# Kernel tuning notes

Hardware: AMD Instinct MI355X
Metric: run time of the kernel (lower is better)

## Reference

```python
import jax, jax.numpy as jnp
import numpy as np

DIM = 3072
NUM_HEADS = 24
HEAD_DIM = 128
INNER = NUM_HEADS * HEAD_DIM
EPS = 1e-5


def _layernorm(x, eps=EPS):
    # affine-free LayerNorm over the last (head_dim) axis
    mu = jnp.mean(x, axis=-1, keepdims=True)
    var = jnp.mean(jnp.square(x - mu), axis=-1, keepdims=True)
    return (x - mu) * jax.lax.rsqrt(var + eps)


def _rope_interleaved(x, cos, sin):
    # x: (B, S_img, H, D); cos/sin: (S_img, D//2). Non-neox (interleaved) style.
    x1 = x[..., 0::2]
    x2 = x[..., 1::2]
    c = cos[None, :, None, :]
    s = sin[None, :, None, :]
    o1 = x1 * c - x2 * s
    o2 = x2 * c + x1 * s
    return jnp.stack([o1, o2], axis=-1).reshape(x.shape)


def setup_inputs() -> dict:
    key = jax.random.key(0)
    ks = jax.random.split(key, 8)
    B, S_txt, S_img = 1, 256, 2048
    hidden_states = jax.random.normal(ks[0], (B, S_img, DIM), dtype=jnp.float32)
    encoder_hidden_states = jax.random.normal(ks[1], (B, S_txt, DIM), dtype=jnp.float32)
    cos = jax.random.uniform(ks[2], (S_img, HEAD_DIM // 2), dtype=jnp.float32)
    sin = jax.random.uniform(ks[3], (S_img, HEAD_DIM // 2), dtype=jnp.float32)
    Wqkv = jax.random.normal(ks[4], (DIM, 3 * INNER), dtype=jnp.float32) * (DIM ** -0.5)
    bqkv = jnp.zeros((3 * INNER,), dtype=jnp.float32)
    Wout = jax.random.normal(ks[5], (INNER, DIM), dtype=jnp.float32) * (INNER ** -0.5)
    bout = jnp.zeros((DIM,), dtype=jnp.float32)
    return {
        "hidden_states": hidden_states,
        "encoder_hidden_states": encoder_hidden_states,
        "cos": cos,
        "sin": sin,
        "Wqkv": Wqkv,
        "bqkv": bqkv,
        "Wout": Wout,
        "bout": bout,
        "text_seq_length": 256,
    }


def reference(hidden_states, encoder_hidden_states, cos, sin, Wqkv, bqkv, Wout, bout, text_seq_length):
    T = text_seq_length
    x = jnp.concatenate([encoder_hidden_states, hidden_states], axis=1)  # (B, S, dim)
    B, S, _ = x.shape
    qkv = x @ Wqkv + bqkv  # (B, S, 3*inner)
    q, k, v = jnp.split(qkv, 3, axis=-1)
    q = q.reshape(B, S, NUM_HEADS, HEAD_DIM)
    k = k.reshape(B, S, NUM_HEADS, HEAD_DIM)
    v = v.reshape(B, S, NUM_HEADS, HEAD_DIM)
    q = _layernorm(q)
    k = _layernorm(k)
    # partial RoPE: only on image-token slice
    q = jnp.concatenate([q[:, :T], _rope_interleaved(q[:, T:], cos, sin)], axis=1)
    k = jnp.concatenate([k[:, :T], _rope_interleaved(k[:, T:], cos, sin)], axis=1)
    scale = 1.0 / (HEAD_DIM ** 0.5)
    scores = jnp.einsum("bqhd,bkhd->bhqk", q, k) * scale
    probs = jax.nn.softmax(scores, axis=-1)
    out = jnp.einsum("bhqk,bkhd->bqhd", probs, v)
    out = out.reshape(B, S, INNER)
    out = out @ Wout + bout
    encoder_out = out[:, :T, :]
    hidden_out = out[:, T:, :]
    return (hidden_out, encoder_out)
```

## Files before the change

kernel.cpp:

```cpp
#include <hip/hip_runtime.h>

#define DIMC 3072
#define NH 24
#define HD 128
#define QKV_N 9216
#define S_TXT 256
#define S_IMG 2048
#define S_TOT 2304

typedef _Float16 f16x8 __attribute__((ext_vector_type(8)));
typedef _Float16 f16x4 __attribute__((ext_vector_type(4)));
typedef _Float16 f16x2 __attribute__((ext_vector_type(2)));
typedef float f32x4 __attribute__((ext_vector_type(4)));

#define MFMA(A, B, C) __builtin_amdgcn_mfma_f32_16x16x32_f16(A, B, C, 0, 0, 0)

#define QSCALE (0.08838834764831845f * 1.4426950408889634f)

__device__ __forceinline__ void gl2lds16(const _Float16* g, _Float16* l) {
    __builtin_amdgcn_global_load_lds(
        (const __attribute__((address_space(1))) unsigned int*)g,
        (__attribute__((address_space(3))) unsigned int*)l,
        16, 0, 0);
}

__global__ __launch_bounds__(256) void split_x(
    const float* __restrict__ enc, const float* __restrict__ hid,
    _Float16* __restrict__ xh)
{
    const int s = blockIdx.x;
    const float* src = (s < S_TXT) ? enc + (size_t)s * DIMC
                                   : hid + (size_t)(s - S_TXT) * DIMC;
    const int t = threadIdx.x;
#pragma unroll
    for (int it = 0; it < 3; ++it) {
        const int i = (it * 256 + t) * 4;
        float4 v = *(const float4*)(src + i);
        f16x4 hv;
        hv.x = (_Float16)v.x; hv.y = (_Float16)v.y;
        hv.z = (_Float16)v.z; hv.w = (_Float16)v.w;
        *(f16x4*)(xh + (size_t)s * DIMC + i) = hv;
    }
}

__global__ __launch_bounds__(256) void transpose_w_hi(
    const float* __restrict__ W, const int ldw, _Float16* __restrict__ Th)
{
    __shared__ float T[64][68];
    const int n0 = blockIdx.x * 64, k0 = blockIdx.y * 64;
    const int t = threadIdx.x;
    {
        const int r = t >> 2, c4 = (t & 3) * 16;
#pragma unroll
        for (int j = 0; j < 4; ++j) {
            float4 v = *(const float4*)(W + (size_t)(k0 + r) * ldw + n0 + c4 + j * 4);
            *(float4*)&T[r][c4 + j * 4] = v;
        }
    }
    __syncthreads();
    const int nr = t >> 2, kp = (t & 3) * 16;
    f16x8 hv0, hv1;
#pragma unroll
    for (int j = 0; j < 8; ++j) hv0[j] = (_Float16)T[kp + j][nr];
#pragma unroll
    for (int j = 0; j < 8; ++j) hv1[j] = (_Float16)T[kp + 8 + j][nr];
    _Float16* dh = Th + (size_t)(n0 + nr) * DIMC + k0 + kp;
    *(f16x8*)(dh) = hv0; *(f16x8*)(dh + 8) = hv1;
}

template <int REMAP>
__global__ __launch_bounds__(256) void gemm_f16_lds(
    const _Float16* __restrict__ Ah, const _Float16* __restrict__ Bh,
    const float* __restrict__ bias, float* __restrict__ C,
    const int nblk_m, const int ldc)
{
    __shared__ __attribute__((aligned(16))) _Float16 Ash[128 * 32];
    __shared__ __attribute__((aligned(16))) _Float16 Bsh[128 * 32];

    const int cpx = (int)gridDim.x >> 3;
    const int wgid = (blockIdx.x & 7) * cpx + (blockIdx.x >> 3);
    const int bm = (wgid % nblk_m) * 128;
    const int bn = (wgid / nblk_m) * 128;

    const int tid = threadIdx.x;
    const int l = tid & 63, w = tid >> 6;
    const int wr = w >> 1, wc = w & 1;
    const int lr = l & 15, g = l >> 4;

    const int srow0 = w * 32 + (l >> 2);
    const int srow1 = srow0 + 16;
    const int skp0 = (((l & 3) ^ ((srow0 >> 1) & 3)) * 8);
    const int skp1 = (((l & 3) ^ ((srow1 >> 1) & 3)) * 8);
    const _Float16* gA0 = Ah + (size_t)(bm + srow0) * DIMC + skp0;
    const _Float16* gA1 = Ah + (size_t)(bm + srow1) * DIMC + skp1;
    const _Float16* gB0 = Bh + (size_t)(bn + srow0) * DIMC + skp0;
    const _Float16* gB1 = Bh + (size_t)(bn + srow1) * DIMC + skp1;
    _Float16* lA0 = &Ash[(w * 32) * 32];
    _Float16* lA1 = &Ash[(w * 32 + 16) * 32];
    _Float16* lB0 = &Bsh[(w * 32) * 32];
    _Float16* lB1 = &Bsh[(w * 32 + 16) * 32];

    int aoff[4], boff[4];
#pragma unroll
    for (int i = 0; i < 4; ++i) {
        const int ra = wr * 64 + i * 16 + lr;
        const int rb = wc * 64 + i * 16 + lr;
        aoff[i] = ra * 32 + ((g ^ ((ra >> 1) & 3)) * 8);
        boff[i] = rb * 32 + ((g ^ ((rb >> 1) & 3)) * 8);
    }

    f32x4 acc[4][4] = {};

    for (int k0 = 0; k0 < DIMC; k0 += 32) {
        gl2lds16(gA0 + k0, lA0);
        gl2lds16(gA1 + k0, lA1);
        gl2lds16(gB0 + k0, lB0);
        gl2lds16(gB1 + k0, lB1);
        __syncthreads();

        f16x8 bhf[4];
#pragma unroll
        for (int ni = 0; ni < 4; ++ni)
            bhf[ni] = *(const f16x8*)&Bsh[boff[ni]];
#pragma unroll
        for (int mi = 0; mi < 4; ++mi) {
            f16x8 ahf = *(const f16x8*)&Ash[aoff[mi]];
#pragma unroll
            for (int ni = 0; ni < 4; ++ni)
                acc[mi][ni] = MFMA(ahf, bhf[ni], acc[mi][ni]);
        }
        __syncthreads();
    }

#pragma unroll
    for (int mi = 0; mi < 4; ++mi)
#pragma unroll
        for (int ni = 0; ni < 4; ++ni) {
            const int cl = bn + wc * 64 + ni * 16 + lr;
            const float bv = bias[cl];
#pragma unroll
            for (int e = 0; e < 4; ++e) {
                const int r = bm + wr * 64 + mi * 16 + g * 4 + e;
                if (REMAP) {
                    const int gr = (r < S_TXT) ? (S_IMG + r) : (r - S_TXT);
                    C[(size_t)gr * DIMC + cl] = acc[mi][ni][e] + bv;
                } else {
                    C[(size_t)r * ldc + cl] = acc[mi][ni][e] + bv;
                }
            }
        }
}

__global__ __launch_bounds__(256) void ln_rope_split(
    const float* __restrict__ qkv,
    const float* __restrict__ cost, const float* __restrict__ sint,
    _Float16* __restrict__ Qh, _Float16* __restrict__ Kh)
{
    const int wave = threadIdx.x >> 6;
    const int lane = threadIdx.x & 63;
    const int task = blockIdx.x * 4 + wave;
    const int s = task / 48;
    const int rem = task % 48;
    const int qk = rem / 24;
    const int h = rem % 24;

    const float* p = qkv + (size_t)s * QKV_N + qk * DIMC + h * HD;
    float2 x = *(const float2*)(p + lane * 2);

    float sum = x.x + x.y;
    float sq = x.x * x.x + x.y * x.y;
#pragma unroll
    for (int off = 1; off < 64; off <<= 1) {
        sum += __shfl_xor(sum, off, 64);
        sq  += __shfl_xor(sq, off, 64);
    }
    const float mu = sum * (1.0f / 128.0f);
    const float var = sq * (1.0f / 128.0f) - mu * mu;
    const float rstd = rsqrtf(var + 1e-5f);
    float y0 = (x.x - mu) * rstd;
    float y1 = (x.y - mu) * rstd;

    if (s >= S_TXT) {
        const int ip = s - S_TXT;
        const float c = cost[ip * 64 + lane];
        const float sn = sint[ip * 64 + lane];
        const float o0 = y0 * c - y1 * sn;
        const float o1 = y1 * c + y0 * sn;
        y0 = o0; y1 = o1;
    }
    if (qk == 0) { y0 *= QSCALE; y1 *= QSCALE; }

    const size_t off = ((size_t)h * S_TOT + s) * HD + lane * 2;
    f16x2 hv; hv.x = (_Float16)y0; hv.y = (_Float16)y1;
    *(f16x2*)((qk ? Kh : Qh) + off) = hv;
}

__global__ __launch_bounds__(256) void v_split_transpose(
    const float* __restrict__ qkv, _Float16* __restrict__ Vth)
{
    __shared__ float T[64][132];
    const int h = blockIdx.y;
    const int s0 = blockIdx.x * 64;
    const int t = threadIdx.x;
    {
        const int sl = t >> 2, dp = (t & 3) * 32;
#pragma unroll
        for (int j = 0; j < 8; ++j) {
            float4 v = *(const float4*)(qkv + (size_t)(s0 + sl) * QKV_N + 2 * DIMC + h * HD + dp + j * 4);
            *(float4*)&T[sl][dp + j * 4] = v;
        }
    }
    __syncthreads();
    const int d = t >> 1, sh = (t & 1) * 32;
    f16x8 hv[4];
#pragma unroll
    for (int ss = 0; ss < 32; ++ss)
        hv[ss >> 3][ss & 7] = (_Float16)T[sh + ss][d];
    _Float16* bh = Vth + ((size_t)h * HD + d) * S_TOT + s0 + sh;
#pragma unroll
    for (int j = 0; j < 4; ++j)
        *(f16x8*)(bh + j * 8) = hv[j];
}

__global__ __launch_bounds__(512) void attn_mfma(
    const _Float16* __restrict__ Qg, const _Float16* __restrict__ Kg,
    const _Float16* __restrict__ Vg, _Float16* __restrict__ aoh)
{
    __shared__ __attribute__((aligned(16))) _Float16 Ksh[4 * 64 * 32];
    __shared__ __attribute__((aligned(16))) _Float16 Vsh[128 * 64];
    __shared__ __attribute__((aligned(16))) _Float16 Pah[8 * 16 * 64];

    const int wgid = ((int)blockIdx.x & 7) * 54 + ((int)blockIdx.x >> 3);
    const int h = wgid / 18;
    const int q0 = (wgid % 18) * 128;
    const int tid = threadIdx.x;
    const int w = tid >> 6, l = tid & 63;
    const int lr = l & 15, g = l >> 4;

    const int qrow = q0 + w * 16 + lr;
    const _Float16* qb = Qg + ((size_t)h * S_TOT + qrow) * HD + g * 8;
    f16x8 qh[4];
#pragma unroll
    for (int db = 0; db < 4; ++db)
        qh[db] = *(const f16x8*)(qb + db * 32);

    f32x4 o[8] = {};
    float mrow = -3.0e38f, lrow = 0.0f;

    const int kxr = (lr >> 1) & 3;
    const int px  = lr & 7;
    int ksl[4];
#pragma unroll
    for (int db = 0; db < 4; ++db) ksl[db] = (g ^ kxr ^ db) * 8;
    const int vs0 = (g ^ px) * 8;
    const int vs1 = ((4 + g) ^ px) * 8;

    const int kkv = tid >> 3, kd = tid & 7;
    const int kdb = kd >> 1, kg0 = (kd & 1) * 2;
    const int kx = (kkv >> 1) & 3;
    const int kbase = kdb * 2048 + kkv * 32;
    const int vd = tid >> 2, vh = tid & 3;
    const int vx = vd & 7;
    const int vbase = vd * 64;
    const int vg0 = vh * 2;
    const _Float16* gK = Kg + ((size_t)h * S_TOT + kkv) * HD + kd * 16;
    const _Float16* gV = Vg + ((size_t)h * HD + vd) * S_TOT + vh * 16;

    uint4 rK0, rK1, rV0, rV1;
#define LOADKV(kv0) { \
    rK0 = *(const uint4*)(gK + (size_t)(kv0) * HD);     rK1 = *(const uint4*)(gK + (size_t)(kv0) * HD + 8); \
    rV0 = *(const uint4*)(gV + (kv0));                  rV1 = *(const uint4*)(gV + (kv0) + 8); }

    LOADKV(0);

    for (int kb = 0; kb < S_TOT / 64; ++kb) {
        __syncthreads();
        *(uint4*)&Ksh[kbase + (((kg0 + 0) ^ kx ^ kdb) * 8)] = rK0;
        *(uint4*)&Ksh[kbase + (((kg0 + 1) ^ kx ^ kdb) * 8)] = rK1;
        *(uint4*)&Vsh[vbase + (((vg0 + 0) ^ vx) * 8)] = rV0;
        *(uint4*)&Vsh[vbase + (((vg0 + 1) ^ vx) * 8)] = rV1;
        __syncthreads();
        if (kb + 1 < S_TOT / 64) LOADKV((kb + 1) * 64);

        f32x4 sT[4] = {};
        __builtin_amdgcn_s_setprio(1);
#pragma unroll
        for (int db = 0; db < 4; ++db)
#pragma unroll
            for (int mf = 0; mf < 4; ++mf) {
                f16x8 kf = *(const f16x8*)&Ksh[db * 2048 + (mf * 16 + lr) * 32 + ksl[db]];
                sT[mf] = MFMA(kf, qh[db], sT[mf]);
            }
        __builtin_amdgcn_s_setprio(0);

        float pm = -3.0e38f;
#pragma unroll
        for (int mf = 0; mf < 4; ++mf)
#pragma unroll
            for (int e = 0; e < 4; ++e)
                pm = fmaxf(pm, sT[mf][e]);
        pm = fmaxf(pm, __shfl_xor(pm, 16, 64));
        pm = fmaxf(pm, __shfl_xor(pm, 32, 64));

        if (__any(pm > mrow + 11.0f)) {
            const float mnew = fmaxf(mrow, pm);
            const float alpha = exp2f(mrow - mnew);
            lrow *= alpha;
            mrow = mnew;
            const float a0 = __shfl(alpha, g * 4 + 0, 64);
            const float a1 = __shfl(alpha, g * 4 + 1, 64);
            const float a2 = __shfl(alpha, g * 4 + 2, 64);
            const float a3 = __shfl(alpha, g * 4 + 3, 64);
#pragma unroll
            for (int df = 0; df < 8; ++df) {
                o[df][0] *= a0; o[df][1] *= a1; o[df][2] *= a2; o[df][3] *= a3;
            }
        }

        float rs = 0.0f;
        float ex_[4][4];
#pragma unroll
        for (int mf = 0; mf < 4; ++mf)
#pragma unroll
            for (int e = 0; e < 4; ++e) {
                const float pv = exp2f(sT[mf][e] - mrow);
                ex_[mf][e] = pv;
                rs += pv;
            }
        rs += __shfl_xor(rs, 16, 64);
        rs += __shfl_xor(rs, 32, 64);
        lrow += rs;

        {
            const int pbase = w * 1024 + lr * 64;
#pragma unroll
            for (int mf = 0; mf < 4; ++mf) {
                const int slot = ((mf * 2 + (g >> 1)) ^ px) * 8 + (g & 1) * 4;
                f16x2 t0; t0.x = (_Float16)ex_[mf][0]; t0.y = (_Float16)ex_[mf][1];
                f16x2 t1; t1.x = (_Float16)ex_[mf][2]; t1.y = (_Float16)ex_[mf][3];
                *(f16x2*)&Pah[pbase + slot]     = t0;
                *(f16x2*)&Pah[pbase + slot + 2] = t1;
            }
        }

        f16x8 pa0 = *(const f16x8*)&Pah[w * 1024 + lr * 64 + vs0];
        f16x8 pa1 = *(const f16x8*)&Pah[w * 1024 + lr * 64 + vs1];
        __builtin_amdgcn_s_setprio(1);
#pragma unroll
        for (int df = 0; df < 8; ++df) {
            f16x8 vf0 = *(const f16x8*)&Vsh[(df * 16 + lr) * 64 + vs0];
            f16x8 vf1 = *(const f16x8*)&Vsh[(df * 16 + lr) * 64 + vs1];
            o[df] = MFMA(pa0, vf0, o[df]);
            o[df] = MFMA(pa1, vf1, o[df]);
        }
        __builtin_amdgcn_s_setprio(0);
    }
#undef LOADKV

    const float inv = 1.0f / lrow;
    const float b0 = __shfl(inv, g * 4 + 0, 64);
    const float b1 = __shfl(inv, g * 4 + 1, 64);
    const float b2 = __shfl(inv, g * 4 + 2, 64);
    const float b3 = __shfl(inv, g * 4 + 3, 64);
    const float bb[4] = {b0, b1, b2, b3};
#pragma unroll
    for (int df = 0; df < 8; ++df)
#pragma unroll
        for (int e = 0; e < 4; ++e) {
            const int r = q0 + w * 16 + g * 4 + e;
            aoh[(size_t)r * DIMC + h * HD + df * 16 + lr] = (_Float16)(o[df][e] * bb[e]);
        }
}

extern "C" void kernel_launch(void* const* d_in, const int* in_sizes, int n_in,
                              void* d_out, int out_size, void* d_ws, size_t ws_size,
                              hipStream_t stream)
{
    const float* hid  = (const float*)d_in[0];
    const float* enc  = (const float*)d_in[1];
    const float* cost = (const float*)d_in[2];
    const float* sint = (const float*)d_in[3];
    const float* Wqkv = (const float*)d_in[4];
    const float* bqkv = (const float*)d_in[5];
    const float* Wout = (const float*)d_in[6];
    const float* bout = (const float*)d_in[7];
    float* out = (float*)d_out;

    char* ws = (char*)d_ws;
    float*    qkv  = (float*)(ws + 0);
    _Float16* aoh  = (_Float16*)(ws + 0);
    _Float16* xh   = (_Float16*)(ws + 84934656);
    _Float16* Qh   = (_Float16*)(ws + 84934656);
    _Float16* Kh   = (_Float16*)(ws + 99090432);
    _Float16* Wth  = (_Float16*)(ws + 113246208);
    _Float16* Vth  = (_Float16*)(ws + 113246208);
    _Float16* W2h  = (_Float16*)(ws + 132120576);

    split_x<<<S_TOT, 256, 0, stream>>>(enc, hid, xh);
    transpose_w_hi<<<dim3(144, 48), 256, 0, stream>>>(Wqkv, QKV_N, Wth);
    gemm_f16_lds<0><<<18 * 72, 256, 0, stream>>>(xh, Wth, bqkv, qkv, 18, QKV_N);
    transpose_w_hi<<<dim3(48, 48), 256, 0, stream>>>(Wout, DIMC, W2h);
    ln_rope_split<<<(S_TOT * 48) / 4, 256, 0, stream>>>(qkv, cost, sint, Qh, Kh);
    v_split_transpose<<<dim3(36, 24), 256, 0, stream>>>(qkv, Vth);
    attn_mfma<<<432, 512, 0, stream>>>(Qh, Kh, Vth, aoh);
    gemm_f16_lds<1><<<18 * 24, 256, 0, stream>>>(aoh, W2h, bout, out, 18, DIMC);
}
```

Measured before the change: 411.3 us.

## Fuse QKV split and V transpose into GEMM epilogue writing fp16

The QKV GEMM epilogue now writes Q and K as fp16 in head-major layout and V transposed, instead of writing a full fp32 qkv buffer. The separate V transpose kernel is removed, and LayerNorm plus RoPE now runs in place on the fp16 Q and K. This removes the fp32 write and re-read of roughly 85MB of intermediate data. In exchange, LayerNorm statistics are computed from fp16-rounded values, which adds precision loss, and the scattered 2-byte epilogue stores for Q and K may coalesce poorly.

```diff
diff --git a/kernel.cpp b/kernel.cpp
--- a/kernel.cpp
+++ b/kernel.cpp
@@ -68,19 +68,19 @@
     *(f16x8*)(dh) = hv0; *(f16x8*)(dh + 8) = hv1;
 }
 
-template <int REMAP>
-__global__ __launch_bounds__(256) void gemm_f16_lds(
+__global__ __launch_bounds__(256) void gemm_qkv(
     const _Float16* __restrict__ Ah, const _Float16* __restrict__ Bh,
-    const float* __restrict__ bias, float* __restrict__ C,
-    const int nblk_m, const int ldc)
+    const float* __restrict__ bias,
+    _Float16* __restrict__ Qh, _Float16* __restrict__ Kh,
+    _Float16* __restrict__ Vt)
 {
     __shared__ __attribute__((aligned(16))) _Float16 Ash[128 * 32];
     __shared__ __attribute__((aligned(16))) _Float16 Bsh[128 * 32];
 
     const int cpx = (int)gridDim.x >> 3;
     const int wgid = (blockIdx.x & 7) * cpx + (blockIdx.x >> 3);
-    const int bm = (wgid % nblk_m) * 128;
-    const int bn = (wgid / nblk_m) * 128;
+    const int bm = (wgid % 18) * 128;
+    const int bn = (wgid / 18) * 128;
 
     const int tid = threadIdx.x;
     const int l = tid & 63, w = tid >> 6;
@@ -132,6 +132,107 @@
         __syncthreads();
     }
 
+    const int nb = bn >> 7;
+    const int typ = nb / NH;
+    const int h = nb % NH;
+
+    if (typ == 2) {
+#pragma unroll
+        for (int mi = 0; mi < 4; ++mi) {
+            const int sbase = bm + wr * 64 + mi * 16 + g * 4;
+#pragma unroll
+            for (int ni = 0; ni < 4; ++ni) {
+                const int col = wc * 64 + ni * 16 + lr;
+                const float bv = bias[bn + col];
+                f16x4 vv;
+                vv.x = (_Float16)(acc[mi][ni][0] + bv);
+                vv.y = (_Float16)(acc[mi][ni][1] + bv);
+                vv.z = (_Float16)(acc[mi][ni][2] + bv);
+                vv.w = (_Float16)(acc[mi][ni][3] + bv);
+                *(f16x4*)&Vt[((size_t)h * HD + col) * S_TOT + sbase] = vv;
+            }
+        }
+    } else {
+        _Float16* dst = (typ ? Kh : Qh) + (size_t)h * S_TOT * HD;
+#pragma unroll
+        for (int mi = 0; mi < 4; ++mi)
+#pragma unroll
+            for (int ni = 0; ni < 4; ++ni) {
+                const int col = wc * 64 + ni * 16 + lr;
+                const float bv = bias[bn + col];
+#pragma unroll
+                for (int e = 0; e < 4; ++e) {
+                    const int r = bm + wr * 64 + mi * 16 + g * 4 + e;
+                    dst[(size_t)r * HD + col] = (_Float16)(acc[mi][ni][e] + bv);
+                }
+            }
+    }
+}
+
+template <int REMAP>
+__global__ __launch_bounds__(256) void gemm_f16_lds(
+    const _Float16* __restrict__ Ah, const _Float16* __restrict__ Bh,
+    const float* __restrict__ bias, float* __restrict__ C,
+    const int nblk_m, const int ldc)
+{
+    __shared__ __attribute__((aligned(16))) _Float16 Ash[128 * 32];
+    __shared__ __attribute__((aligned(16))) _Float16 Bsh[128 * 32];
+
+    const int cpx = (int)gridDim.x >> 3;
+    const int wgid = (blockIdx.x & 7) * cpx + (blockIdx.x >> 3);
+    const int bm = (wgid % nblk_m) * 128;
+    const int bn = (wgid / nblk_m) * 128;
+
+    const int tid = threadIdx.x;
+    const int l = tid & 63, w = tid >> 6;
+    const int wr = w >> 1, wc = w & 1;
+    const int lr = l & 15, g = l >> 4;
+
+    const int srow0 = w * 32 + (l >> 2);
+    const int srow1 = srow0 + 16;
+    const int skp0 = (((l & 3) ^ ((srow0 >> 1) & 3)) * 8);
+    const int skp1 = (((l & 3) ^ ((srow1 >> 1) & 3)) * 8);
+    const _Float16* gA0 = Ah + (size_t)(bm + srow0) * DIMC + skp0;
+    const _Float16* gA1 = Ah + (size_t)(bm + srow1) * DIMC + skp1;
+    const _Float16* gB0 = Bh + (size_t)(bn + srow0) * DIMC + skp0;
+    const _Float16* gB1 = Bh + (size_t)(bn + srow1) * DIMC + skp1;
+    _Float16* lA0 = &Ash[(w * 32) * 32];
+    _Float16* lA1 = &Ash[(w * 32 + 16) * 32];
+    _Float16* lB0 = &Bsh[(w * 32) * 32];
+    _Float16* lB1 = &Bsh[(w * 32 + 16) * 32];
+
+    int aoff[4], boff[4];
+#pragma unroll
+    for (int i = 0; i < 4; ++i) {
+        const int ra = wr * 64 + i * 16 + lr;
+        const int rb = wc * 64 + i * 16 + lr;
+        aoff[i] = ra * 32 + ((g ^ ((ra >> 1) & 3)) * 8);
+        boff[i] = rb * 32 + ((g ^ ((rb >> 1) & 3)) * 8);
+    }
+
+    f32x4 acc[4][4] = {};
+
+    for (int k0 = 0; k0 < DIMC; k0 += 32) {
+        gl2lds16(gA0 + k0, lA0);
+        gl2lds16(gA1 + k0, lA1);
+        gl2lds16(gB0 + k0, lB0);
+        gl2lds16(gB1 + k0, lB1);
+        __syncthreads();
+
+        f16x8 bhf[4];
+#pragma unroll
+        for (int ni = 0; ni < 4; ++ni)
+            bhf[ni] = *(const f16x8*)&Bsh[boff[ni]];
+#pragma unroll
+        for (int mi = 0; mi < 4; ++mi) {
+            f16x8 ahf = *(const f16x8*)&Ash[aoff[mi]];
+#pragma unroll
+            for (int ni = 0; ni < 4; ++ni)
+                acc[mi][ni] = MFMA(ahf, bhf[ni], acc[mi][ni]);
+        }
+        __syncthreads();
+    }
+
 #pragma unroll
     for (int mi = 0; mi < 4; ++mi)
 #pragma unroll
@@ -151,10 +252,9 @@
         }
 }
 
-__global__ __launch_bounds__(256) void ln_rope_split(
-    const float* __restrict__ qkv,
-    const float* __restrict__ cost, const float* __restrict__ sint,
-    _Float16* __restrict__ Qh, _Float16* __restrict__ Kh)
+__global__ __launch_bounds__(256) void ln_rope_inplace(
+    _Float16* __restrict__ Qh, _Float16* __restrict__ Kh,
+    const float* __restrict__ cost, const float* __restrict__ sint)
 {
     const int wave = threadIdx.x >> 6;
     const int lane = threadIdx.x & 63;
@@ -164,11 +264,12 @@
     const int qk = rem / 24;
     const int h = rem % 24;
 
-    const float* p = qkv + (size_t)s * QKV_N + qk * DIMC + h * HD;
-    float2 x = *(const float2*)(p + lane * 2);
-
-    float sum = x.x + x.y;
-    float sq = x.x * x.x + x.y * x.y;
+    _Float16* p = (qk ? Kh : Qh) + ((size_t)h * S_TOT + s) * HD + lane * 2;
+    f16x2 xv = *(const f16x2*)p;
+    float x0 = (float)xv.x, x1 = (float)xv.y;
+
+    float sum = x0 + x1;
+    float sq = x0 * x0 + x1 * x1;
 #pragma unroll
     for (int off = 1; off < 64; off <<= 1) {
         sum += __shfl_xor(sum, off, 64);
@@ -177,8 +278,8 @@
     const float mu = sum * (1.0f / 128.0f);
     const float var = sq * (1.0f / 128.0f) - mu * mu;
     const float rstd = rsqrtf(var + 1e-5f);
-    float y0 = (x.x - mu) * rstd;
-    float y1 = (x.y - mu) * rstd;
+    float y0 = (x0 - mu) * rstd;
+    float y1 = (x1 - mu) * rstd;
 
     if (s >= S_TXT) {
         const int ip = s - S_TXT;
@@ -190,36 +291,8 @@
     }
     if (qk == 0) { y0 *= QSCALE; y1 *= QSCALE; }
 
-    const size_t off = ((size_t)h * S_TOT + s) * HD + lane * 2;
     f16x2 hv; hv.x = (_Float16)y0; hv.y = (_Float16)y1;
-    *(f16x2*)((qk ? Kh : Qh) + off) = hv;
-}
-
-__global__ __launch_bounds__(256) void v_split_transpose(
-    const float* __restrict__ qkv, _Float16* __restrict__ Vth)
-{
-    __shared__ float T[64][132];
-    const int h = blockIdx.y;
-    const int s0 = blockIdx.x * 64;
-    const int t = threadIdx.x;
-    {
-        const int sl = t >> 2, dp = (t & 3) * 32;
-#pragma unroll
-        for (int j = 0; j < 8; ++j) {
-            float4 v = *(const float4*)(qkv + (size_t)(s0 + sl) * QKV_N + 2 * DIMC + h * HD + dp + j * 4);
-            *(float4*)&T[sl][dp + j * 4] = v;
-        }
-    }
-    __syncthreads();
-    const int d = t >> 1, sh = (t & 1) * 32;
-    f16x8 hv[4];
-#pragma unroll
-    for (int ss = 0; ss < 32; ++ss)
-        hv[ss >> 3][ss & 7] = (_Float16)T[sh + ss][d];
-    _Float16* bh = Vth + ((size_t)h * HD + d) * S_TOT + s0 + sh;
-#pragma unroll
-    for (int j = 0; j < 4; ++j)
-        *(f16x8*)(bh + j * 8) = hv[j];
+    *(f16x2*)p = hv;
 }
 
 __global__ __launch_bounds__(512) void attn_mfma(
@@ -387,21 +460,19 @@
     float* out = (float*)d_out;
 
     char* ws = (char*)d_ws;
-    float*    qkv  = (float*)(ws + 0);
-    _Float16* aoh  = (_Float16*)(ws + 0);
-    _Float16* xh   = (_Float16*)(ws + 84934656);
-    _Float16* Qh   = (_Float16*)(ws + 84934656);
-    _Float16* Kh   = (_Float16*)(ws + 99090432);
-    _Float16* Wth  = (_Float16*)(ws + 113246208);
-    _Float16* Vth  = (_Float16*)(ws + 113246208);
-    _Float16* W2h  = (_Float16*)(ws + 132120576);
+    _Float16* Qh  = (_Float16*)(ws + 0);
+    _Float16* Kh  = (_Float16*)(ws + 14155776);
+    _Float16* Vth = (_Float16*)(ws + 28311552);
+    _Float16* aoh = (_Float16*)(ws + 42467328);
+    _Float16* xh  = (_Float16*)(ws + 56623104);
+    _Float16* Wth = (_Float16*)(ws + 70778880);
+    _Float16* W2h = (_Float16*)(ws + 127401984);
 
     split_x<<<S_TOT, 256, 0, stream>>>(enc, hid, xh);
     transpose_w_hi<<<dim3(144, 48), 256, 0, stream>>>(Wqkv, QKV_N, Wth);
-    gemm_f16_lds<0><<<18 * 72, 256, 0, stream>>>(xh, Wth, bqkv, qkv, 18, QKV_N);
+    gemm_qkv<<<18 * 72, 256, 0, stream>>>(xh, Wth, bqkv, Qh, Kh, Vth);
     transpose_w_hi<<<dim3(48, 48), 256, 0, stream>>>(Wout, DIMC, W2h);
-    ln_rope_split<<<(S_TOT * 48) / 4, 256, 0, stream>>>(qkv, cost, sint, Qh, Kh);
-    v_split_transpose<<<dim3(36, 24), 256, 0, stream>>>(qkv, Vth);
+    ln_rope_inplace<<<(S_TOT * 48) / 4, 256, 0, stream>>>(Qh, Kh, cost, sint);
     attn_mfma<<<432, 512, 0, stream>>>(Qh, Kh, Vth, aoh);
     gemm_f16_lds<1><<<18 * 24, 256, 0, stream>>>(aoh, W2h, bout, out, 18, DIMC);
 }
```

After: 399.7 us. 2.8% less time.
